# Kernel tuning notes

Hardware: AMD Instinct MI355X
Metric: run time of the kernel (lower is better)

The kernel has to match this reference:

```python
import jax, jax.numpy as jnp
import numpy as np

KERNEL_SIZE = 9
DOMAIN = 8
VTH1 = 1.0
VTH2 = 1.0
VTH3 = 100000.0
BETA1 = min(0.999, 0.9)
BETA2 = min(0.999, 0.9)
BETA3 = min(0.999, 0.95)


def _make_kernels() -> np.ndarray:
    # 16 oriented Gaussian kernels, sigma1=1, sigma2=4, phi = k*2*pi/32, k=0..15
    ks = []
    a = np.linspace(-DOMAIN, DOMAIN, KERNEL_SIZE)
    xs, ys = np.meshgrid(a, a, indexing='xy')  # centered at (0,0)
    coo = np.stack([xs, ys], axis=2)  # [K,K,2]
    l1, l2 = 1.0 ** 2, 4.0 ** 2
    for count in range(16):
        phi = count * 2.0 * np.pi / 32.0
        c, s = np.cos(phi), np.sin(phi)
        cxx = l1 * c * c + l2 * s * s
        cxy = (l1 - l2) * c * s
        cyy = l1 * s * s + l2 * c * c
        cov = np.array([[cxx, cxy], [cxy, cyy]])
        ci = np.linalg.inv(cov)
        cd = np.linalg.det(cov)
        frac = 1.0 / (2.0 * np.pi * np.sqrt(cd))
        # quadratic form: (-coo) @ ci . coo  (matches torch einsum chain)
        q = np.einsum('xyj,jk,xyk->xy', -coo, ci, coo)
        ks.append(frac * np.exp(q / 2.0))
    return np.stack(ks).astype(np.float32)[:, None]  # [16,1,9,9]


def heaviside(v):
    return (v > 0).astype(v.dtype)


def setup_inputs() -> dict:
    key = jax.random.key(0)
    k1, k2, k3 = jax.random.split(key, 3)
    B, T, H, W = 16, 50, 64, 64
    x = jax.random.uniform(k1, (B, T, 1, H, W), dtype=jnp.float32)
    kernels = jnp.asarray(_make_kernels())  # [16,1,9,9], fixed buffer
    fan1 = 16 * H * W
    w1 = jax.random.uniform(k2, (200, fan1), jnp.float32, -1.0, 1.0) / np.sqrt(fan1)
    w2 = jax.random.uniform(k3, (1, 200), jnp.float32, -1.0, 1.0) / np.sqrt(200.0)
    return {"x": x, "kernels": kernels, "w1": w1, "w2": w2}


def reference(x, kernels, w1, w2):
    B, T, C, H, W = x.shape
    pad = KERNEL_SIZE // 2

    def step(carry, xt):
        m1, m2, m3 = carry
        # conv2d, stride 1, same padding -> [B,16,H,W]
        g1 = jax.lax.conv_general_dilated(
            xt, kernels, window_strides=(1, 1),
            padding=[(pad, pad), (pad, pad)],
            dimension_numbers=('NCHW', 'OIHW', 'NCHW'))
        # snntorch Leaky, reset_mechanism='zero': reset from previous mem,
        # then mem = (beta*mem + input) * (1 - reset); spk = H(mem - vth)
        r1 = heaviside(m1 - VTH1)
        m1 = (BETA1 * m1 + g1) * (1.0 - r1)
        z1 = heaviside(m1 - VTH1)
        g2 = z1.reshape(B, -1) @ w1.T  # [B,200]
        r2 = heaviside(m2 - VTH2)
        m2 = (BETA2 * m2 + g2) * (1.0 - r2)
        z2 = heaviside(m2 - VTH2)
        g3 = z2 @ w2.T  # [B,1]
        r3 = heaviside(m3 - VTH3)  # threshold 1e5: never fires
        m3 = (BETA3 * m3 + g3) * (1.0 - r3)
        return (m1, m2, m3), m3

    m1 = jnp.zeros((B, 16, H, W), x.dtype)
    m2 = jnp.zeros((B, 200), x.dtype)
    m3 = jnp.zeros((B, 1), x.dtype)
    xt = jnp.moveaxis(x, 1, 0)  # [T,B,1,H,W]
    _, ys = jax.lax.scan(step, (m1, m2, m3), xt)
    return jnp.moveaxis(ys, 0, 1)  # [B,T,1]
```

## Files before the change

kernel.cpp:

```cpp
#include <hip/hip_runtime.h>
#include <hip/hip_bf16.h>


typedef __attribute__((ext_vector_type(8))) short short8;
typedef __attribute__((ext_vector_type(4))) float f32x4;
typedef __attribute__((ext_vector_type(4))) int   i32x4;

#define B_   16
#define T_   50
#define HW_  4096
#define K1N  65536
#define M_   800
#define N2_  200
#define NP_  256
#define KSPL 32
#define BM2  128
#define BK2  64
#define KCH  (K1N / KSPL)
#define MT2  7
#define SW   84
#define TILE (12 * SW)
#define NCONV 512
#define NPERM (200 * 32)

static __device__ __forceinline__ short8 mk8(uint a, uint b, uint c, uint d){
  union { uint u[4]; short8 v; } x;
  x.u[0] = a; x.u[1] = b; x.u[2] = c; x.u[3] = d;
  return x.v;
}
static __device__ __forceinline__ uint fnl(uint a, uint b){ return (a >> 16) | (b << 16); }

template<bool WODD>
static __device__ __forceinline__ void rd5(const uint* p, int dw, uint e[5]){
  if (WODD){
    e[0] = p[dw];
    uint2 a = *(const uint2*)(p + dw + 1);
    uint2 b = *(const uint2*)(p + dw + 3);
    e[1] = a.x; e[2] = a.y; e[3] = b.x; e[4] = b.y;
  } else {
    uint2 a = *(const uint2*)(p + dw);
    uint2 b = *(const uint2*)(p + dw + 2);
    e[0] = a.x; e[1] = a.y; e[2] = b.x; e[3] = b.y;
    e[4] = p[dw + 4];
  }
}

template<bool WODD>
static __device__ __forceinline__ void conv_phase(const uint* T0, const uint* T1,
                                                  int bdw,
                                                  const short8 (&afh)[5],
                                                  const short8 (&afl)[5],
                                                  f32x4& acc0, f32x4& acc1){
  #pragma unroll
  for (int ks = 0; ks < 5; ++ks){
    const int dw = bdw + (SW / 2) * 2 * ks;
    uint h[5], m[5];
    rd5<WODD>(T0, dw, h);
    rd5<WODD>(T1, dw, m);
    short8 bh0 = mk8(h[0], h[1], h[2], h[3]);
    short8 bm0 = mk8(m[0], m[1], m[2], m[3]);
    acc0 = __builtin_amdgcn_mfma_f32_16x16x32_bf16(afh[ks], bh0, acc0, 0, 0, 0);
    acc0 = __builtin_amdgcn_mfma_f32_16x16x32_bf16(afh[ks], bm0, acc0, 0, 0, 0);
    acc0 = __builtin_amdgcn_mfma_f32_16x16x32_bf16(afl[ks], bh0, acc0, 0, 0, 0);
    short8 bh1 = mk8(fnl(h[0], h[1]), fnl(h[1], h[2]), fnl(h[2], h[3]), fnl(h[3], h[4]));
    short8 bm1 = mk8(fnl(m[0], m[1]), fnl(m[1], m[2]), fnl(m[2], m[3]), fnl(m[3], m[4]));
    acc1 = __builtin_amdgcn_mfma_f32_16x16x32_bf16(afh[ks], bh1, acc1, 0, 0, 0);
    acc1 = __builtin_amdgcn_mfma_f32_16x16x32_bf16(afh[ks], bm1, acc1, 0, 0, 0);
    acc1 = __builtin_amdgcn_mfma_f32_16x16x32_bf16(afl[ks], bh1, acc1, 0, 0, 0);
  }
}

static __device__ __forceinline__ void stage_tile(ushort* Th, ushort* Tm,
                                                  int eb, float4 f){
  float vv[4] = {f.x, f.y, f.z, f.w};
  ushort sh[4], sm[4];
  #pragma unroll
  for (int ii = 0; ii < 4; ++ii){
    __hip_bfloat16 h = __float2bfloat16(vv[ii]);
    float t1 = vv[ii] - __bfloat162float(h);
    __hip_bfloat16 m = __float2bfloat16(t1);
    sh[ii] = *reinterpret_cast<ushort*>(&h);
    sm[ii] = *reinterpret_cast<ushort*>(&m);
  }
  *(ushort4*)(Th + eb) = make_ushort4(sh[0], sh[1], sh[2], sh[3]);
  *(ushort4*)(Tm + eb) = make_ushort4(sm[0], sm[1], sm[2], sm[3]);
}

__global__ __launch_bounds__(256) void k01_fused(const float* __restrict__ x,
                                                 const float* __restrict__ kern,
                                                 const float* __restrict__ w1,
                                                 unsigned char* __restrict__ zout,
                                                 char* __restrict__ wa,
                                                 char* __restrict__ wb){
  __shared__ __align__(16) ushort smem[9152];
  const int bid = blockIdx.x;
  const int tid = threadIdx.x;

  if (bid >= NCONV){
    uint* la = (uint*)smem;
    uint* lb = ((uint*)smem) + 528;
    const int bid2 = bid - NCONV;
    const int n = bid2 >> 5;
    const int strip = bid2 & 31;
    const int p128 = tid & 127;
    const int qp   = tid >> 7;
    const int o = p128 & 7, s = p128 >> 3;
    const float* src = w1 + (size_t)n * K1N + strip * 128 + p128;
    #pragma unroll
    for (int qi = 0; qi < 2; ++qi){
      const int q = 2 * qp + qi;
      uint ua = 0, ub = 0;
      #pragma unroll
      for (int r = 0; r < 4; ++r){
        float v = src[(size_t)(4 * q + r) * 4096];
        float af = rintf(v * 16384.f);
        float rr = v - af * 0x1p-14f;
        float bf = rintf(rr * 0x1p22f);
        int A = (int)af, Bq = (int)bf;
        if (Bq == 128){ A += 1; Bq = -128; }
        ua |= ((uint)(A & 255))  << (8 * r);
        ub |= ((uint)(Bq & 255)) << (8 * r);
      }
      const int u = 64 * o + 4 * s + q + o;
      la[u] = ua;
      lb[u] = ub;
    }
    __syncthreads();
    {
      const int j0 = 2 * tid;
      const int o2 = j0 >> 6;
      uint a0 = la[j0 + o2], a1 = la[j0 + 1 + o2];
      uint b0 = lb[j0 + o2], b1 = lb[j0 + 1 + o2];
      const size_t ob = (size_t)n * K1N + strip * 2048 + (size_t)j0 * 4;
      *(uint2*)(wa + ob) = make_uint2(a0, a1);
      *(uint2*)(wb + ob) = make_uint2(b0, b1);
    }
    return;
  }

  ushort* Ah  = smem;
  ushort* Alo = smem + 2560;
  ushort* Tt  = smem + 5120;

  const int strip = bid & 31;
  const int b = bid >> 5;
  const int w = tid >> 6;
  const int l = tid & 63;
  const int q = l >> 4;
  const int s = l & 15;

  for (int slot = tid; slot < 16 * 160; slot += 256){
    int ch = slot / 160, kk = slot - ch * 160;
    int dy = kk >> 4, dx = kk & 15;
    float v = 0.f;
    if (dy < 9 && dx < 9) v = kern[ch * 81 + dy * 9 + dx];
    __hip_bfloat16 h = __float2bfloat16(v);
    float hf = __bfloat162float(h);
    __hip_bfloat16 lo = __float2bfloat16(v - hf);
    Ah[slot]  = *reinterpret_cast<ushort*>(&h);
    Alo[slot] = *reinterpret_cast<ushort*>(&lo);
  }

  const bool sact = tid < 240;
  const int sr = tid / 20, sc4 = tid - sr * 20;
  const int r0 = 2 * strip - 4;
  const int imr = r0 + sr;
  const bool sin = sact && imr >= 0 && imr < 64 && sc4 >= 1 && sc4 <= 16;
  const float* xb = x + (size_t)b * (T_ * HW_);
  const float* xsrc = xb + (sin ? (imr * 64 + (sc4 - 1) * 4) : 0);
  const int eb = sr * SW + sc4 * 4;

  {
    float4 f0 = make_float4(0.f, 0.f, 0.f, 0.f);
    if (sin) f0 = *(const float4*)(xsrc);
    if (sact) stage_tile(Tt + 0 * TILE, Tt + 1 * TILE, eb, f0);
  }
  __syncthreads();

  short8 afh[5], afl[5];
  #pragma unroll
  for (int ks = 0; ks < 5; ++ks){
    afh[ks] = *(const short8*)(Ah + s * 160 + ks * 32 + q * 8);
    afl[ks] = *(const short8*)(Alo + s * 160 + ks * 32 + q * 8);
  }

  const int p0 = (s >> 3) + (q >> 1);
  const int bdw = 42 * p0 + 4 * (s & 7) + 4 * (q & 1) + w;
  const bool wodd = (w & 1) != 0;

  float m1v[2][4];
  #pragma unroll
  for (int oi = 0; oi < 2; ++oi)
    #pragma unroll
    for (int r = 0; r < 4; ++r) m1v[oi][r] = 0.f;

  for (int t = 0; t < T_; ++t){
    __syncthreads();
    float4 nfx = make_float4(0.f, 0.f, 0.f, 0.f);
    if (t + 1 < T_ && sin) nfx = *(const float4*)(xsrc + (size_t)(t + 1) * HW_);

    const int bb = t & 1;
    const uint* T0 = (const uint*)(Tt + (bb * 2 + 0) * TILE);
    const uint* T1 = (const uint*)(Tt + (bb * 2 + 1) * TILE);
    f32x4 acc0 = (f32x4)(0.f), acc1 = (f32x4)(0.f);
    if (wodd) conv_phase<true >(T0, T1, bdw, afh, afl, acc0, acc1);
    else      conv_phase<false>(T0, T1, bdw, afh, afl, acc0, acc1);

    const size_t zr = ((size_t)(t * B_ + b)) * K1N + strip * 2048 + s * 16 + q * 4;
    {
      uint zw = 0;
      #pragma unroll
      for (int r = 0; r < 4; ++r){
        float m = m1v[0][r];
        float nm = (m > 1.0f) ? 0.0f : __fadd_rn(__fmul_rn(0.9f, m), acc0[r]);
        m1v[0][r] = nm;
        if (nm > 1.0f) zw |= (1u << (8 * r));
      }
      *(uint*)(zout + zr + (size_t)(2 * w) * 256) = zw;
    }
    {
      uint zw = 0;
      #pragma unroll
      for (int r = 0; r < 4; ++r){
        float m = m1v[1][r];
        float nm = (m > 1.0f) ? 0.0f : __fadd_rn(__fmul_rn(0.9f, m), acc1[r]);
        m1v[1][r] = nm;
        if (nm > 1.0f) zw |= (1u << (8 * r));
      }
      *(uint*)(zout + zr + (size_t)(2 * w + 1) * 256) = zw;
    }

    if (t + 1 < T_ && sact)
      stage_tile(Tt + ((bb ^ 1) * 2 + 0) * TILE, Tt + ((bb ^ 1) * 2 + 1) * TILE, eb, nfx);
  }
}

static __device__ __forceinline__ void k2_load(const unsigned char* __restrict__ z,
                                               const char* __restrict__ wa,
                                               const char* __restrict__ wb,
                                               int m0, int kg, int tid,
                                               uint4& pa, uint4 pb[4]){
  {
    int row = tid >> 2, c16 = tid & 3;
    int m = m0 + row;
    pa = make_uint4(0, 0, 0, 0);
    if (m < M_) pa = *(const uint4*)(z + (size_t)m * K1N + kg + c16 * 16);
  }
  #pragma unroll
  for (int i = 0; i < 4; ++i){
    int idx = tid + 512 * i;
    int g   = idx >> 2;
    int c16 = idx & 3;
    int sel = g >> 8;
    int r   = g & 255;
    const char* src = sel ? wb : wa;
    pb[i] = make_uint4(0, 0, 0, 0);
    if (r < N2_) pb[i] = *(const uint4*)(src + (size_t)r * K1N + kg + c16 * 16);
  }
}

__global__ __launch_bounds__(512) void k2_gemm(const unsigned char* __restrict__ z,
                                               const char* __restrict__ wa,
                                               const char* __restrict__ wb,
                                               float* __restrict__ P){
  __shared__ __align__(16) unsigned char Al[128 * 80];
  __shared__ __align__(16) unsigned char Bw[512 * 80];

  const int bid = blockIdx.x;
  const int L = (bid & 7) * 28 + (bid >> 3);
  const int ks = L / MT2;
  const int mt = L % MT2;
  const int m0 = mt * BM2;
  const int k0 = ks * KCH;
  const int tid = threadIdx.x;
  const int wv = tid >> 6;
  const int mh = wv >> 2;
  const int nq = wv & 3;
  const int l  = tid & 63;
  const int lr = l & 15;
  const int lq = l >> 4;

  const i32x4 zero4 = {0, 0, 0, 0};
  i32x4 accA[4][4], accB[4][4];
  #pragma unroll
  for (int mf = 0; mf < 4; ++mf)
    #pragma unroll
    for (int nf = 0; nf < 4; ++nf){ accA[mf][nf] = zero4; accB[mf][nf] = zero4; }

  uint4 pa, pb[4];
  k2_load(z, wa, wb, m0, k0, tid, pa, pb);

  #pragma unroll 1
  for (int kc = 0; kc < KCH; kc += BK2){
    {
      int row = tid >> 2, c16 = tid & 3;
      *(uint4*)(Al + row * 80 + c16 * 16) = pa;
    }
    #pragma unroll
    for (int i = 0; i < 4; ++i){
      int idx = tid + 512 * i;
      int g   = idx >> 2;
      int c16 = idx & 3;
      *(uint4*)(Bw + g * 80 + c16 * 16) = pb[i];
    }
    __syncthreads();

    if (kc + BK2 < KCH) k2_load(z, wa, wb, m0, k0 + kc + BK2, tid, pa, pb);

    i32x4 af[4], ba[4], bbf[4];
    #pragma unroll
    for (int mf = 0; mf < 4; ++mf)
      af[mf] = *(const i32x4*)(Al + (mh * 64 + mf * 16 + lr) * 80 + lq * 16);
    #pragma unroll
    for (int nf = 0; nf < 4; ++nf){
      ba[nf]  = *(const i32x4*)(Bw + (nq * 64 + nf * 16 + lr) * 80 + lq * 16);
      bbf[nf] = *(const i32x4*)(Bw + (256 + nq * 64 + nf * 16 + lr) * 80 + lq * 16);
    }
    #pragma unroll
    for (int mf = 0; mf < 4; ++mf)
      #pragma unroll
      for (int nf = 0; nf < 4; ++nf){
        accA[mf][nf] = __builtin_amdgcn_mfma_i32_16x16x64_i8(af[mf], ba[nf],  accA[mf][nf], 0, 0, 0);
        accB[mf][nf] = __builtin_amdgcn_mfma_i32_16x16x64_i8(af[mf], bbf[nf], accB[mf][nf], 0, 0, 0);
      }
    __syncthreads();
  }

  #pragma unroll
  for (int mf = 0; mf < 4; ++mf)
    #pragma unroll
    for (int nf = 0; nf < 4; ++nf)
      #pragma unroll
      for (int r = 0; r < 4; ++r){
        int m = m0 + mh * 64 + mf * 16 + lq * 4 + r;
        int n = nq * 64 + nf * 16 + lr;
        if (m < M_ && n < N2_)
          P[((size_t)ks * M_ + m) * N2_ + n] =
            fmaf((float)accA[mf][nf][r], 0x1p-14f, (float)accB[mf][nf][r] * 0x1p-22f);
      }
}

__global__ __launch_bounds__(256) void k2b_reduce(const float* __restrict__ P,
                                                  float* __restrict__ G2){
  int j = blockIdx.x * 256 + threadIdx.x;
  if (j >= M_ * N2_) return;
  float s = 0.f;
  #pragma unroll
  for (int ks = 0; ks < KSPL; ++ks) s += P[(size_t)ks * (M_ * N2_) + j];
  G2[j] = s;
}

__global__ __launch_bounds__(256) void k3_scan(const float* __restrict__ G2,
                                               const float* __restrict__ w2,
                                               float* __restrict__ out){
  const int b = blockIdx.x;
  const int tid = threadIdx.x;
  const float w = (tid < N2_) ? w2[tid] : 0.f;
  float m2 = 0.f, m3 = 0.f;
  __shared__ float part[4];

  float nxt = (tid < N2_) ? G2[(size_t)b * N2_ + tid] : 0.f;
  for (int t = 0; t < T_; ++t){
    float g2v = nxt;
    if (t < T_ - 1 && tid < N2_) nxt = G2[(size_t)((t + 1) * B_ + b) * N2_ + tid];
    float nm = (m2 > 1.0f) ? 0.f : __fadd_rn(__fmul_rn(0.9f, m2), g2v);
    m2 = nm;
    float s = (m2 > 1.0f) ? w : 0.f;
    #pragma unroll
    for (int off = 32; off > 0; off >>= 1) s += __shfl_down(s, off, 64);
    if ((tid & 63) == 0) part[tid >> 6] = s;
    __syncthreads();
    if (tid == 0){
      float g3 = (part[0] + part[1]) + (part[2] + part[3]);
      m3 = __fadd_rn(__fmul_rn(0.95f, m3), g3);
      out[b * T_ + t] = m3;
    }
    __syncthreads();
  }
}

extern "C" void kernel_launch(void* const* d_in, const int* in_sizes, int n_in,
                              void* d_out, int out_size, void* d_ws, size_t ws_size,
                              hipStream_t stream){
  const float* x    = (const float*)d_in[0];
  const float* kern = (const float*)d_in[1];
  const float* w1   = (const float*)d_in[2];
  const float* w2   = (const float*)d_in[3];
  float* out = (float*)d_out;

  char* p = (char*)d_ws;
  unsigned char* z8 = (unsigned char*)p;     p += (size_t)M_ * K1N;
  char* wa = p;                              p += (size_t)NP_ * K1N;
  char* wb = p;                              p += (size_t)NP_ * K1N;
  float* P  = (float*)p;                     p += (size_t)KSPL * M_ * N2_ * 4;
  float* G2 = (float*)p;                     p += (size_t)M_ * N2_ * 4;

  size_t need = (size_t)(p - (char*)d_ws);
  if (ws_size < need) return;

  hipLaunchKernelGGL(k01_fused,  dim3(NCONV + NPERM), dim3(256), 0, stream,
                     x, kern, w1, z8, wa, wb);
  hipLaunchKernelGGL(k2_gemm,    dim3(MT2 * KSPL), dim3(512), 0, stream, z8, wa, wb, P);
  hipLaunchKernelGGL(k2b_reduce, dim3((M_ * N2_ + 255) / 256), dim3(256), 0, stream, P, G2);
  hipLaunchKernelGGL(k3_scan,    dim3(B_), dim3(256), 0, stream, G2, w2, out);
}
```

Baseline: 129.6 us.

## Interleave hi/lo bf16 tile and compute four column groups per wave

```diff
diff --git a/kernel.cpp b/kernel.cpp
--- a/kernel.cpp
+++ b/kernel.cpp
@@ -18,9 +18,10 @@
 #define BK2  64
 #define KCH  (K1N / KSPL)
 #define MT2  7
-#define SW   84
-#define TILE (12 * SW)
-#define NCONV 512
+#define RS   84
+#define TR13 13
+#define TILEU (TR13 * RS)
+#define NCONV 256
 #define NPERM (200 * 32)
 
 static __device__ __forceinline__ short8 mk8(uint a, uint b, uint c, uint d){
@@ -28,62 +29,43 @@
   x.u[0] = a; x.u[1] = b; x.u[2] = c; x.u[3] = d;
   return x.v;
 }
-static __device__ __forceinline__ uint fnl(uint a, uint b){ return (a >> 16) | (b << 16); }
-
-template<bool WODD>
-static __device__ __forceinline__ void rd5(const uint* p, int dw, uint e[5]){
-  if (WODD){
-    e[0] = p[dw];
-    uint2 a = *(const uint2*)(p + dw + 1);
-    uint2 b = *(const uint2*)(p + dw + 3);
-    e[1] = a.x; e[2] = a.y; e[3] = b.x; e[4] = b.y;
-  } else {
-    uint2 a = *(const uint2*)(p + dw);
-    uint2 b = *(const uint2*)(p + dw + 2);
-    e[0] = a.x; e[1] = a.y; e[2] = b.x; e[3] = b.y;
-    e[4] = p[dw + 4];
-  }
-}
-
-template<bool WODD>
-static __device__ __forceinline__ void conv_phase(const uint* T0, const uint* T1,
-                                                  int bdw,
-                                                  const short8 (&afh)[5],
-                                                  const short8 (&afl)[5],
-                                                  f32x4& acc0, f32x4& acc1){
+
+static __device__ __forceinline__ void conv_phase4(const uint* __restrict__ T,
+                                                   int bdw,
+                                                   const short8 (&afh)[5],
+                                                   const short8 (&afl)[5],
+                                                   f32x4 (&acc)[4]){
   #pragma unroll
   for (int ks = 0; ks < 5; ++ks){
-    const int dw = bdw + (SW / 2) * 2 * ks;
-    uint h[5], m[5];
-    rd5<WODD>(T0, dw, h);
-    rd5<WODD>(T1, dw, m);
-    short8 bh0 = mk8(h[0], h[1], h[2], h[3]);
-    short8 bm0 = mk8(m[0], m[1], m[2], m[3]);
-    acc0 = __builtin_amdgcn_mfma_f32_16x16x32_bf16(afh[ks], bh0, acc0, 0, 0, 0);
-    acc0 = __builtin_amdgcn_mfma_f32_16x16x32_bf16(afh[ks], bm0, acc0, 0, 0, 0);
-    acc0 = __builtin_amdgcn_mfma_f32_16x16x32_bf16(afl[ks], bh0, acc0, 0, 0, 0);
-    short8 bh1 = mk8(fnl(h[0], h[1]), fnl(h[1], h[2]), fnl(h[2], h[3]), fnl(h[3], h[4]));
-    short8 bm1 = mk8(fnl(m[0], m[1]), fnl(m[1], m[2]), fnl(m[2], m[3]), fnl(m[3], m[4]));
-    acc1 = __builtin_amdgcn_mfma_f32_16x16x32_bf16(afh[ks], bh1, acc1, 0, 0, 0);
-    acc1 = __builtin_amdgcn_mfma_f32_16x16x32_bf16(afh[ks], bm1, acc1, 0, 0, 0);
-    acc1 = __builtin_amdgcn_mfma_f32_16x16x32_bf16(afl[ks], bh1, acc1, 0, 0, 0);
-  }
-}
-
-static __device__ __forceinline__ void stage_tile(ushort* Th, ushort* Tm,
-                                                  int eb, float4 f){
-  float vv[4] = {f.x, f.y, f.z, f.w};
-  ushort sh[4], sm[4];
-  #pragma unroll
-  for (int ii = 0; ii < 4; ++ii){
-    __hip_bfloat16 h = __float2bfloat16(vv[ii]);
-    float t1 = vv[ii] - __bfloat162float(h);
-    __hip_bfloat16 m = __float2bfloat16(t1);
-    sh[ii] = *reinterpret_cast<ushort*>(&h);
-    sm[ii] = *reinterpret_cast<ushort*>(&m);
-  }
-  *(ushort4*)(Th + eb) = make_ushort4(sh[0], sh[1], sh[2], sh[3]);
-  *(ushort4*)(Tm + eb) = make_ushort4(sm[0], sm[1], sm[2], sm[3]);
+    const uint* p = T + bdw + 2 * RS * ks;
+    uint4 a = *(const uint4*)(p);
+    uint4 b = *(const uint4*)(p + 4);
+    uint4 c = *(const uint4*)(p + 8);
+    uint u[12] = {a.x, a.y, a.z, a.w, b.x, b.y, b.z, b.w, c.x, c.y, c.z, c.w};
+    uint lo[10], hi[10];
+    #pragma unroll
+    for (int i = 0; i < 10; ++i){
+      lo[i] = __builtin_amdgcn_perm(u[i + 1], u[i], 0x05040100);
+      hi[i] = __builtin_amdgcn_perm(u[i + 1], u[i], 0x07060302);
+    }
+    #pragma unroll
+    for (int j = 0; j < 4; ++j){
+      short8 bh = mk8(lo[j], lo[j + 2], lo[j + 4], lo[j + 6]);
+      short8 bm = mk8(hi[j], hi[j + 2], hi[j + 4], hi[j + 6]);
+      acc[j] = __builtin_amdgcn_mfma_f32_16x16x32_bf16(afh[ks], bh, acc[j], 0, 0, 0);
+      acc[j] = __builtin_amdgcn_mfma_f32_16x16x32_bf16(afh[ks], bm, acc[j], 0, 0, 0);
+      acc[j] = __builtin_amdgcn_mfma_f32_16x16x32_bf16(afl[ks], bh, acc[j], 0, 0, 0);
+    }
+  }
+}
+
+static __device__ __forceinline__ uint pack_px(float v){
+  __hip_bfloat16 h = __float2bfloat16(v);
+  float t1 = v - __bfloat162float(h);
+  __hip_bfloat16 m = __float2bfloat16(t1);
+  uint uh = *reinterpret_cast<ushort*>(&h);
+  uint um = *reinterpret_cast<ushort*>(&m);
+  return (um << 16) | uh;
 }
 
 __global__ __launch_bounds__(256) void k01_fused(const float* __restrict__ x,
@@ -92,13 +74,13 @@
                                                  unsigned char* __restrict__ zout,
                                                  char* __restrict__ wa,
                                                  char* __restrict__ wb){
-  __shared__ __align__(16) ushort smem[9152];
+  __shared__ __align__(16) uint smem[4744];
   const int bid = blockIdx.x;
   const int tid = threadIdx.x;
 
   if (bid >= NCONV){
-    uint* la = (uint*)smem;
-    uint* lb = ((uint*)smem) + 528;
+    uint* la = smem;
+    uint* lb = smem + 528;
     const int bid2 = bid - NCONV;
     const int n = bid2 >> 5;
     const int strip = bid2 & 31;
@@ -138,42 +120,50 @@
     return;
   }
 
-  ushort* Ah  = smem;
-  ushort* Alo = smem + 2560;
-  ushort* Tt  = smem + 5120;
-
-  const int strip = bid & 31;
-  const int b = bid >> 5;
-  const int w = tid >> 6;
-  const int l = tid & 63;
-  const int q = l >> 4;
-  const int s = l & 15;
+  ushort* Ah  = (ushort*)smem;
+  ushort* Alo = (ushort*)smem + 2560;
+  uint*   Tt  = smem + 2560;
+
+  const int u16 = bid & 15;
+  const int b   = bid >> 4;
+  const int wv = tid >> 6;
+  const int h  = wv >> 1;
+  const int w  = wv & 1;
+  const int l  = tid & 63;
+  const int q  = l >> 4;
+  const int s  = l & 15;
 
   for (int slot = tid; slot < 16 * 160; slot += 256){
     int ch = slot / 160, kk = slot - ch * 160;
     int dy = kk >> 4, dx = kk & 15;
     float v = 0.f;
     if (dy < 9 && dx < 9) v = kern[ch * 81 + dy * 9 + dx];
-    __hip_bfloat16 h = __float2bfloat16(v);
-    float hf = __bfloat162float(h);
+    __hip_bfloat16 hh = __float2bfloat16(v);
+    float hf = __bfloat162float(hh);
     __hip_bfloat16 lo = __float2bfloat16(v - hf);
-    Ah[slot]  = *reinterpret_cast<ushort*>(&h);
+    Ah[slot]  = *reinterpret_cast<ushort*>(&hh);
     Alo[slot] = *reinterpret_cast<ushort*>(&lo);
+  }
+  for (int j = tid; j < 2 * RS; j += 256){
+    int bf = j / RS, cc = j - bf * RS;
+    Tt[bf * TILEU + 12 * RS + cc] = 0u;
   }
 
   const bool sact = tid < 240;
   const int sr = tid / 20, sc4 = tid - sr * 20;
-  const int r0 = 2 * strip - 4;
-  const int imr = r0 + sr;
+  const int imr = 4 * u16 - 4 + sr;
   const bool sin = sact && imr >= 0 && imr < 64 && sc4 >= 1 && sc4 <= 16;
   const float* xb = x + (size_t)b * (T_ * HW_);
   const float* xsrc = xb + (sin ? (imr * 64 + (sc4 - 1) * 4) : 0);
-  const int eb = sr * SW + sc4 * 4;
+  const int eb = sr * RS + sc4 * 4;
 
   {
     float4 f0 = make_float4(0.f, 0.f, 0.f, 0.f);
     if (sin) f0 = *(const float4*)(xsrc);
-    if (sact) stage_tile(Tt + 0 * TILE, Tt + 1 * TILE, eb, f0);
+    if (sact){
+      uint4 pk = make_uint4(pack_px(f0.x), pack_px(f0.y), pack_px(f0.z), pack_px(f0.w));
+      *(uint4*)(Tt + eb) = pk;
+    }
   }
   __syncthreads();
 
@@ -184,15 +174,15 @@
     afl[ks] = *(const short8*)(Alo + s * 160 + ks * 32 + q * 8);
   }
 
-  const int p0 = (s >> 3) + (q >> 1);
-  const int bdw = 42 * p0 + 4 * (s & 7) + 4 * (q & 1) + w;
-  const bool wodd = (w & 1) != 0;
-
-  float m1v[2][4];
-  #pragma unroll
-  for (int oi = 0; oi < 2; ++oi)
-    #pragma unroll
-    for (int r = 0; r < 4; ++r) m1v[oi][r] = 0.f;
+  const int p0  = (s >> 3) + (q >> 1);
+  const int bdw = (2 * h + p0) * RS + 8 * (s & 7) + 8 * (q & 1) + 4 * w;
+  const int S   = 2 * u16 + h;
+
+  float m1v[4][4];
+  #pragma unroll
+  for (int j = 0; j < 4; ++j)
+    #pragma unroll
+    for (int r = 0; r < 4; ++r) m1v[j][r] = 0.f;
 
   for (int t = 0; t < T_; ++t){
     __syncthreads();
@@ -200,38 +190,29 @@
     if (t + 1 < T_ && sin) nfx = *(const float4*)(xsrc + (size_t)(t + 1) * HW_);
 
     const int bb = t & 1;
-    const uint* T0 = (const uint*)(Tt + (bb * 2 + 0) * TILE);
-    const uint* T1 = (const uint*)(Tt + (bb * 2 + 1) * TILE);
-    f32x4 acc0 = (f32x4)(0.f), acc1 = (f32x4)(0.f);
-    if (wodd) conv_phase<true >(T0, T1, bdw, afh, afl, acc0, acc1);
-    else      conv_phase<false>(T0, T1, bdw, afh, afl, acc0, acc1);
-
-    const size_t zr = ((size_t)(t * B_ + b)) * K1N + strip * 2048 + s * 16 + q * 4;
-    {
+    f32x4 acc[4];
+    #pragma unroll
+    for (int j = 0; j < 4; ++j) acc[j] = (f32x4)(0.f);
+    conv_phase4(Tt + bb * TILEU, bdw, afh, afl, acc);
+
+    const size_t zr = ((size_t)(t * B_ + b)) * K1N + (size_t)S * 2048 + s * 16 + q * 4;
+    #pragma unroll
+    for (int j = 0; j < 4; ++j){
       uint zw = 0;
       #pragma unroll
       for (int r = 0; r < 4; ++r){
-        float m = m1v[0][r];
-        float nm = (m > 1.0f) ? 0.0f : __fadd_rn(__fmul_rn(0.9f, m), acc0[r]);
-        m1v[0][r] = nm;
+        float m = m1v[j][r];
+        float nm = (m > 1.0f) ? 0.0f : __fadd_rn(__fmul_rn(0.9f, m), acc[j][r]);
+        m1v[j][r] = nm;
         if (nm > 1.0f) zw |= (1u << (8 * r));
       }
-      *(uint*)(zout + zr + (size_t)(2 * w) * 256) = zw;
-    }
-    {
-      uint zw = 0;
-      #pragma unroll
-      for (int r = 0; r < 4; ++r){
-        float m = m1v[1][r];
-        float nm = (m > 1.0f) ? 0.0f : __fadd_rn(__fmul_rn(0.9f, m), acc1[r]);
-        m1v[1][r] = nm;
-        if (nm > 1.0f) zw |= (1u << (8 * r));
-      }
-      *(uint*)(zout + zr + (size_t)(2 * w + 1) * 256) = zw;
-    }
-
-    if (t + 1 < T_ && sact)
-      stage_tile(Tt + ((bb ^ 1) * 2 + 0) * TILE, Tt + ((bb ^ 1) * 2 + 1) * TILE, eb, nfx);
+      *(uint*)(zout + zr + (size_t)(4 * w + j) * 256) = zw;
+    }
+
+    if (t + 1 < T_ && sact){
+      uint4 pk = make_uint4(pack_px(nfx.x), pack_px(nfx.y), pack_px(nfx.z), pack_px(nfx.w));
+      *(uint4*)(Tt + (bb ^ 1) * TILEU + eb) = pk;
+    }
   }
 }
 
```

After: 133.7 us. +3.2%, slower.

## Double-buffer B tile in LDS and load A fragments directly from global

Applied to the files above, without the earlier changes.

```diff
diff --git a/kernel.cpp b/kernel.cpp
--- a/kernel.cpp
+++ b/kernel.cpp
@@ -235,17 +235,9 @@
   }
 }
 
-static __device__ __forceinline__ void k2_load(const unsigned char* __restrict__ z,
-                                               const char* __restrict__ wa,
-                                               const char* __restrict__ wb,
-                                               int m0, int kg, int tid,
-                                               uint4& pa, uint4 pb[4]){
-  {
-    int row = tid >> 2, c16 = tid & 3;
-    int m = m0 + row;
-    pa = make_uint4(0, 0, 0, 0);
-    if (m < M_) pa = *(const uint4*)(z + (size_t)m * K1N + kg + c16 * 16);
-  }
+static __device__ __forceinline__ void k2_loadB(const char* __restrict__ wa,
+                                                const char* __restrict__ wb,
+                                                int kg, int tid, uint4 pb[4]){
   #pragma unroll
   for (int i = 0; i < 4; ++i){
     int idx = tid + 512 * i;
@@ -263,8 +255,7 @@
                                                const char* __restrict__ wa,
                                                const char* __restrict__ wb,
                                                float* __restrict__ P){
-  __shared__ __align__(16) unsigned char Al[128 * 80];
-  __shared__ __align__(16) unsigned char Bw[512 * 80];
+  __shared__ __align__(16) unsigned char Bw[2][512 * 80];
 
   const int bid = blockIdx.x;
   const int L = (bid & 7) * 28 + (bid >> 3);
@@ -280,6 +271,14 @@
   const int lr = l & 15;
   const int lq = l >> 4;
 
+  const unsigned char* za[4];
+  #pragma unroll
+  for (int mf = 0; mf < 4; ++mf){
+    int m = m0 + mh * 64 + mf * 16 + lr;
+    if (m >= M_) m = M_ - 1;
+    za[mf] = z + (size_t)m * K1N + k0 + lq * 16;
+  }
+
   const i32x4 zero4 = {0, 0, 0, 0};
   i32x4 accA[4][4], accB[4][4];
   #pragma unroll
@@ -287,34 +286,32 @@
     #pragma unroll
     for (int nf = 0; nf < 4; ++nf){ accA[mf][nf] = zero4; accB[mf][nf] = zero4; }
 
-  uint4 pa, pb[4];
-  k2_load(z, wa, wb, m0, k0, tid, pa, pb);
+  uint4 pb[4];
+  k2_loadB(wa, wb, k0, tid, pb);
+  #pragma unroll
+  for (int i = 0; i < 4; ++i){
+    int idx = tid + 512 * i;
+    int g = idx >> 2, c16 = idx & 3;
+    *(uint4*)(&Bw[0][g * 80 + c16 * 16]) = pb[i];
+  }
 
   #pragma unroll 1
   for (int kc = 0; kc < KCH; kc += BK2){
-    {
-      int row = tid >> 2, c16 = tid & 3;
-      *(uint4*)(Al + row * 80 + c16 * 16) = pa;
-    }
-    #pragma unroll
-    for (int i = 0; i < 4; ++i){
-      int idx = tid + 512 * i;
-      int g   = idx >> 2;
-      int c16 = idx & 3;
-      *(uint4*)(Bw + g * 80 + c16 * 16) = pb[i];
-    }
+    const int cur = (kc >> 6) & 1;
     __syncthreads();
 
-    if (kc + BK2 < KCH) k2_load(z, wa, wb, m0, k0 + kc + BK2, tid, pa, pb);
-
-    i32x4 af[4], ba[4], bbf[4];
+    if (kc + BK2 < KCH) k2_loadB(wa, wb, k0 + kc + BK2, tid, pb);
+
+    i32x4 af[4];
     #pragma unroll
     for (int mf = 0; mf < 4; ++mf)
-      af[mf] = *(const i32x4*)(Al + (mh * 64 + mf * 16 + lr) * 80 + lq * 16);
+      af[mf] = *(const i32x4*)(za[mf] + kc);
+
+    i32x4 ba[4], bbf[4];
     #pragma unroll
     for (int nf = 0; nf < 4; ++nf){
-      ba[nf]  = *(const i32x4*)(Bw + (nq * 64 + nf * 16 + lr) * 80 + lq * 16);
-      bbf[nf] = *(const i32x4*)(Bw + (256 + nq * 64 + nf * 16 + lr) * 80 + lq * 16);
+      ba[nf]  = *(const i32x4*)(&Bw[cur][(nq * 64 + nf * 16 + lr) * 80 + lq * 16]);
+      bbf[nf] = *(const i32x4*)(&Bw[cur][(256 + nq * 64 + nf * 16 + lr) * 80 + lq * 16]);
     }
     #pragma unroll
     for (int mf = 0; mf < 4; ++mf)
@@ -323,7 +320,15 @@
         accA[mf][nf] = __builtin_amdgcn_mfma_i32_16x16x64_i8(af[mf], ba[nf],  accA[mf][nf], 0, 0, 0);
         accB[mf][nf] = __builtin_amdgcn_mfma_i32_16x16x64_i8(af[mf], bbf[nf], accB[mf][nf], 0, 0, 0);
       }
-    __syncthreads();
+
+    if (kc + BK2 < KCH){
+      #pragma unroll
+      for (int i = 0; i < 4; ++i){
+        int idx = tid + 512 * i;
+        int g = idx >> 2, c16 = idx & 3;
+        *(uint4*)(&Bw[cur ^ 1][g * 80 + c16 * 16]) = pb[i];
+      }
+    }
   }
 
   #pragma unroll
```

After: 142.4 us. 9.8% more time.
